# Kernel tuning notes

Hardware: AMD Instinct MI355X
Metric: run time of the kernel (lower is better)

## Reference

```python
import jax, jax.numpy as jnp
import numpy as np

B, T, LATENT, D, N_ENVS = 128, 64, 16, 512, 4
TOPK_RATIO = 0.1
TEMPERATURE = 1.0


def setup_inputs() -> dict:
    key = jax.random.key(0)
    k1, k2, k3, k4 = jax.random.split(key, 4)
    z_s = jax.random.normal(k1, (B, T, LATENT), dtype=jnp.float32)
    env_idx = jax.random.randint(k2, (B,), 0, N_ENVS, dtype=jnp.int64 if jax.config.jax_enable_x64 else jnp.int32)
    A_base = jax.random.normal(k3, (D, D), dtype=jnp.float32) * 0.1
    A_deltas = jax.random.normal(k4, (N_ENVS, D, D), dtype=jnp.float32) * 0.01  # stacked ParameterList
    return {"z_s": z_s, "env_idx": env_idx, "A_base": A_base, "A_deltas": A_deltas}


def reference(z_s, env_idx, A_base, A_deltas):
    b = z_s.shape[0]
    d = A_base.shape[0]
    # Per-env delta add: the torch loop sums delta_e * (env_idx==e) over envs,
    # which (one env per sample) equals a gather of A_deltas at env_idx.
    A_logits = A_base[None, :, :] + A_deltas[env_idx]          # [B, d, d]
    A_soft = jax.nn.sigmoid(A_logits / TEMPERATURE)            # [B, d, d]
    # Batched top-k sparsification (replaces the per-sample python loop).
    k = max(1, int(TOPK_RATIO * d * d))
    flat = A_logits.reshape(b, d * d)                          # [B, d*d]
    topk_vals, topk_idx = jax.lax.top_k(flat, k)               # [B, k]
    rows = jnp.arange(b)[:, None]                              # [B, 1]
    A_flat = jnp.zeros_like(flat).at[rows, topk_idx].set(jax.nn.sigmoid(topk_vals))
    A = A_flat.reshape(b, d, d)
    return A, A_logits, A_soft
```

## Files before the change

kernel.cpp:

```cpp
#include <hip/hip_runtime.h>
#include <stdint.h>

#define D_DIM   512
#define DD      262144
#define DD4     65536
#define B_DIM   128
#define N_ENVS  4
#define K_SEL   26214
#define BDD     33554432u
#define NBLK    64
#define CAP2    65536
#define CAP3    4096

typedef float nfloat4 __attribute__((ext_vector_type(4)));

#define PK_OFF      64
#define CNT_OFF     128
#define HISTP_OFF   4096
#define HISTP_BYTES (NBLK * N_ENVS * 256 * 4)
#define PAIRS_OFF   (512 * 1024)
#define PAIRS_BYTES ((size_t)N_ENVS * CAP2 * 8)
#define SEL_NEED    (PAIRS_OFF + PAIRS_BYTES)

__device__ __forceinline__ uint32_t fkey(float f) {
    uint32_t u = __float_as_uint(f);
    return (u & 0x80000000u) ? ~u : (u | 0x80000000u);
}
__device__ __forceinline__ float sigmoidf_(float x) {
    return 1.0f / (1.0f + __expf(-x));
}

__global__ __launch_bounds__(256) void hist8_kernel(
    const float* __restrict__ base, const float* __restrict__ deltas,
    uint32_t* __restrict__ histp, uint32_t* __restrict__ cnt8)
{
    int e = blockIdx.y;
    const float4* b4 = (const float4*)base;
    const float4* d4 = (const float4*)(deltas + (size_t)e * DD);
    __shared__ uint32_t s_h[256];
    int tid = threadIdx.x;
    s_h[tid] = 0;
    if (blockIdx.x == 0 && tid == 0) cnt8[e] = 0;
    __syncthreads();
    int g0 = blockIdx.x * 256 + tid;
    #pragma unroll
    for (int r = 0; r < 4; ++r) {
        int g = g0 + r * 16384;
        float4 bv = b4[g], dv = d4[g];
        atomicAdd(&s_h[fkey(bv.x + dv.x) >> 24], 1u);
        atomicAdd(&s_h[fkey(bv.y + dv.y) >> 24], 1u);
        atomicAdd(&s_h[fkey(bv.z + dv.z) >> 24], 1u);
        atomicAdd(&s_h[fkey(bv.w + dv.w) >> 24], 1u);
    }
    __syncthreads();
    histp[(blockIdx.x * N_ENVS + e) * 256 + tid] = s_h[tid];
}

__global__ __launch_bounds__(256) void gather8_kernel(
    const float* __restrict__ base, const float* __restrict__ deltas,
    const uint32_t* __restrict__ histp, uint32_t* __restrict__ pk,
    uint32_t* __restrict__ cnt8, uint2* __restrict__ pairs8)
{
    int e = blockIdx.y;
    const float4* b4 = (const float4*)base;
    const float4* d4 = (const float4*)(deltas + (size_t)e * DD);
    uint2* pp = pairs8 + (size_t)e * CAP2;
    __shared__ uint32_t s_h[256];
    __shared__ uint32_t s_scan[256];
    __shared__ uint32_t s_P, s_base;
    int tid = threadIdx.x;

    uint32_t sum = 0;
    #pragma unroll 8
    for (int j = 0; j < NBLK; ++j)
        sum += histp[(j * N_ENVS + e) * 256 + tid];
    s_h[tid] = sum;
    __syncthreads();
    if (tid == 0) {
        uint32_t cum = 0;
        for (int b = 255; b >= 0; --b) {
            uint32_t c = s_h[b];
            if (cum + c >= (uint32_t)K_SEL) {
                s_P = (uint32_t)b;
                if (blockIdx.x == 0) {
                    pk[2 * e + 0] = (uint32_t)b;
                    pk[2 * e + 1] = (uint32_t)K_SEL - cum;
                }
                break;
            }
            cum += c;
        }
    }
    __syncthreads();
    uint32_t P = s_P;

    int g0 = blockIdx.x * 256 + tid;
    uint32_t keys[16];
    uint32_t m = 0;
    #pragma unroll
    for (int r = 0; r < 4; ++r) {
        int g = g0 + r * 16384;
        float4 bv = b4[g], dv = d4[g];
        uint32_t k0 = fkey(bv.x + dv.x), k1 = fkey(bv.y + dv.y);
        uint32_t k2 = fkey(bv.z + dv.z), k3 = fkey(bv.w + dv.w);
        keys[r * 4 + 0] = k0; keys[r * 4 + 1] = k1;
        keys[r * 4 + 2] = k2; keys[r * 4 + 3] = k3;
        m += ((k0 >> 24) == P) + ((k1 >> 24) == P)
           + ((k2 >> 24) == P) + ((k3 >> 24) == P);
    }
    s_scan[tid] = m;
    __syncthreads();
    #pragma unroll
    for (int off = 1; off < 256; off <<= 1) {
        uint32_t v = (tid >= off) ? s_scan[tid - off] : 0u;
        __syncthreads();
        s_scan[tid] += v;
        __syncthreads();
    }
    uint32_t excl = s_scan[tid] - m;
    if (tid == 255) s_base = atomicAdd(&cnt8[e], s_scan[255]);
    __syncthreads();
    uint32_t pos = s_base + excl;

    #pragma unroll
    for (int r = 0; r < 4; ++r) {
        int g = g0 + r * 16384;
        #pragma unroll
        for (int j = 0; j < 4; ++j) {
            uint32_t key = keys[r * 4 + j];
            if ((key >> 24) == P) {
                if (pos < CAP2) pp[pos] = make_uint2(key, (uint32_t)(g * 4 + j));
                ++pos;
            }
        }
    }
}

__global__ __launch_bounds__(1024) void select2_kernel(
    const uint32_t* __restrict__ pk, const uint32_t* __restrict__ cnt8,
    const uint2* __restrict__ pairs8, uint32_t* __restrict__ thrcut)
{
    int e = blockIdx.x;
    const uint2* pp = pairs8 + (size_t)e * CAP2;
    uint32_t M = cnt8[e]; if (M > CAP2) M = CAP2;
    uint32_t krem8 = pk[2 * e + 1];

    __shared__ uint32_t s_h16[256];
    __shared__ uint2    s_pairs[CAP3];
    __shared__ uint32_t s_b16, s_krem16, s_cnt;
    int tid = threadIdx.x;
    if (tid < 256) s_h16[tid] = 0;
    if (tid == 0) s_cnt = 0;
    __syncthreads();

    for (uint32_t j = tid; j < M; j += 1024)
        atomicAdd(&s_h16[(pp[j].x >> 16) & 255u], 1u);
    __syncthreads();
    if (tid == 0) {
        uint32_t cum = 0;
        for (int b = 255; b >= 0; --b) {
            uint32_t c = s_h16[b];
            if (cum + c >= krem8) { s_b16 = (uint32_t)b; s_krem16 = krem8 - cum; break; }
            cum += c;
        }
    }
    __syncthreads();
    uint32_t b16 = s_b16;
    for (uint32_t j = tid; j < M; j += 1024) {
        uint2 p = pp[j];
        if (((p.x >> 16) & 255u) == b16) {
            uint32_t pos = atomicAdd(&s_cnt, 1u);
            if (pos < CAP3) s_pairs[pos] = p;
        }
    }
    __syncthreads();
    uint32_t M2 = s_cnt; if (M2 > CAP3) M2 = CAP3;
    uint32_t target = s_krem16 - 1;
    for (uint32_t j = tid; j < M2; j += 1024) {
        uint2 me = s_pairs[j];
        uint32_t rank = 0;
        for (uint32_t l = 0; l < M2; ++l) {
            uint2 o = s_pairs[l];
            rank += (o.x > me.x) || (o.x == me.x && o.y < me.y);
        }
        if (rank == target) {
            thrcut[2 * e + 0] = me.x;
            thrcut[2 * e + 1] = me.y;
        }
    }
}

__global__ __launch_bounds__(256) void fused_write_kernel(
    const int* __restrict__ env_idx, const float* __restrict__ base,
    const float* __restrict__ deltas, const uint32_t* __restrict__ thrcut,
    float* __restrict__ out)
{
    int b = blockIdx.y;
    int e = env_idx[b];
    uint32_t T = thrcut[2 * e], C = thrcut[2 * e + 1];
    const float4* b4 = (const float4*)base;
    const float4* d4 = (const float4*)(deltas + (size_t)e * DD);
    nfloat4* o4 = (nfloat4*)out + (size_t)b * DD4;
    int g0 = blockIdx.x * 512 + threadIdx.x;
    #pragma unroll
    for (int r = 0; r < 2; ++r) {
        int g = g0 + r * 256;
        uint32_t i0 = (uint32_t)g * 4u;
        float4 bv = b4[g];
        float4 dv = d4[g];
        nfloat4 lg = { bv.x + dv.x, bv.y + dv.y, bv.z + dv.z, bv.w + dv.w };
        nfloat4 sg = { sigmoidf_(lg.x), sigmoidf_(lg.y),
                       sigmoidf_(lg.z), sigmoidf_(lg.w) };
        uint32_t kx = fkey(lg.x), ky = fkey(lg.y), kz = fkey(lg.z), kw = fkey(lg.w);
        nfloat4 av;
        av.x = (kx > T || (kx == T && i0 + 0u <= C)) ? sg.x : 0.0f;
        av.y = (ky > T || (ky == T && i0 + 1u <= C)) ? sg.y : 0.0f;
        av.z = (kz > T || (kz == T && i0 + 2u <= C)) ? sg.z : 0.0f;
        av.w = (kw > T || (kw == T && i0 + 3u <= C)) ? sg.w : 0.0f;
        __builtin_nontemporal_store(av, o4 + g);
        __builtin_nontemporal_store(lg, o4 + g + (BDD / 4));
        __builtin_nontemporal_store(sg, o4 + g + 2ull * (BDD / 4));
    }
}

extern "C" void kernel_launch(void* const* d_in, const int* in_sizes, int n_in,
                              void* d_out, int out_size, void* d_ws, size_t ws_size,
                              hipStream_t stream) {
    const int*   env_idx  = (const int*)d_in[1];
    const float* A_base   = (const float*)d_in[2];
    const float* A_deltas = (const float*)d_in[3];
    float* out = (float*)d_out;

    uint32_t* thrcut = (uint32_t*)d_ws;

    char* scratch;
    if (ws_size >= SEL_NEED) {
        scratch = (char*)d_ws;
    } else {
        size_t out_bytes = (size_t)out_size * sizeof(float);
        scratch = (char*)d_out + ((out_bytes - SEL_NEED) & ~(size_t)255);
    }
    uint32_t* pk     = (uint32_t*)(scratch + PK_OFF);
    uint32_t* cnt8   = (uint32_t*)(scratch + CNT_OFF);
    uint32_t* histp  = (uint32_t*)(scratch + HISTP_OFF);
    uint2*    pairs8 = (uint2*)   (scratch + PAIRS_OFF);

    hist8_kernel  <<<dim3(NBLK, N_ENVS), 256, 0, stream>>>(A_base, A_deltas,
                                                           histp, cnt8);
    gather8_kernel<<<dim3(NBLK, N_ENVS), 256, 0, stream>>>(A_base, A_deltas, histp,
                                                           pk, cnt8, pairs8);
    select2_kernel<<<N_ENVS, 1024, 0, stream>>>(pk, cnt8, pairs8, thrcut);
    fused_write_kernel<<<dim3(DD4 / 512, B_DIM), 256, 0, stream>>>(
        env_idx, A_base, A_deltas, thrcut, out);
}
```

Before: 461.6 us.

## Compute per-env outputs once per element and broadcast to batch rows

The write kernel now computes logits, sigmoid and the masked top-k values for all four environments once per element, then writes them to 16 batch rows per block by switching on env_idx. Before, each of the 128 batch rows reloaded and recomputed its environment's values. The stores switch from nontemporal to regular stores, and the grid becomes 256x8 with a 16-row loop. CAP2 is also enlarged, which raises the scratch footprint. Because the kernel is dominated by 400MB of writes, the savings in reads and compute may matter little, and losing the nontemporal hint could hurt.

```diff
diff --git a/kernel.cpp b/kernel.cpp
--- a/kernel.cpp
+++ b/kernel.cpp
@@ -9,7 +9,7 @@
 #define K_SEL   26214
 #define BDD     33554432u
 #define NBLK    64
-#define CAP2    65536
+#define CAP2    98304
 #define CAP3    4096
 
 typedef float nfloat4 __attribute__((ext_vector_type(4)));
@@ -17,7 +17,6 @@
 #define PK_OFF      64
 #define CNT_OFF     128
 #define HISTP_OFF   4096
-#define HISTP_BYTES (NBLK * N_ENVS * 256 * 4)
 #define PAIRS_OFF   (512 * 1024)
 #define PAIRS_BYTES ((size_t)N_ENVS * CAP2 * 8)
 #define SEL_NEED    (PAIRS_OFF + PAIRS_BYTES)
@@ -190,36 +189,47 @@
     }
 }
 
-__global__ __launch_bounds__(256) void fused_write_kernel(
+__global__ __launch_bounds__(256) void write_bcast_kernel(
     const int* __restrict__ env_idx, const float* __restrict__ base,
     const float* __restrict__ deltas, const uint32_t* __restrict__ thrcut,
     float* __restrict__ out)
 {
-    int b = blockIdx.y;
-    int e = env_idx[b];
-    uint32_t T = thrcut[2 * e], C = thrcut[2 * e + 1];
-    const float4* b4 = (const float4*)base;
-    const float4* d4 = (const float4*)(deltas + (size_t)e * DD);
-    nfloat4* o4 = (nfloat4*)out + (size_t)b * DD4;
-    int g0 = blockIdx.x * 512 + threadIdx.x;
-    #pragma unroll
-    for (int r = 0; r < 2; ++r) {
-        int g = g0 + r * 256;
-        uint32_t i0 = (uint32_t)g * 4u;
-        float4 bv = b4[g];
-        float4 dv = d4[g];
+    int g = blockIdx.x * 256 + threadIdx.x;
+    uint32_t i0 = (uint32_t)g * 4u;
+    float4 bv = ((const float4*)base)[g];
+
+    nfloat4 lgv[N_ENVS], sgv[N_ENVS], avv[N_ENVS];
+    #pragma unroll
+    for (int e = 0; e < N_ENVS; ++e) {
+        float4 dv = ((const float4*)(deltas + (size_t)e * DD))[g];
+        uint32_t T = thrcut[2 * e], C = thrcut[2 * e + 1];
         nfloat4 lg = { bv.x + dv.x, bv.y + dv.y, bv.z + dv.z, bv.w + dv.w };
         nfloat4 sg = { sigmoidf_(lg.x), sigmoidf_(lg.y),
                        sigmoidf_(lg.z), sigmoidf_(lg.w) };
-        uint32_t kx = fkey(lg.x), ky = fkey(lg.y), kz = fkey(lg.z), kw = fkey(lg.w);
+        uint32_t kx = fkey(lg.x), ky = fkey(lg.y);
+        uint32_t kz = fkey(lg.z), kw = fkey(lg.w);
         nfloat4 av;
         av.x = (kx > T || (kx == T && i0 + 0u <= C)) ? sg.x : 0.0f;
         av.y = (ky > T || (ky == T && i0 + 1u <= C)) ? sg.y : 0.0f;
         av.z = (kz > T || (kz == T && i0 + 2u <= C)) ? sg.z : 0.0f;
         av.w = (kw > T || (kw == T && i0 + 3u <= C)) ? sg.w : 0.0f;
-        __builtin_nontemporal_store(av, o4 + g);
-        __builtin_nontemporal_store(lg, o4 + g + (BDD / 4));
-        __builtin_nontemporal_store(sg, o4 + g + 2ull * (BDD / 4));
+        lgv[e] = lg; sgv[e] = sg; avv[e] = av;
+    }
+
+    const int ROWS = B_DIM / 8;
+    int b0 = blockIdx.y * ROWS;
+    nfloat4* o0 = (nfloat4*)out + g;
+    #pragma unroll 4
+    for (int bb = 0; bb < ROWS; ++bb) {
+        int b = b0 + bb;
+        int e = env_idx[b];
+        nfloat4* o = o0 + (size_t)b * DD4;
+        switch (e) {
+        case 0: o[0] = avv[0]; o[BDD/4] = lgv[0]; o[2*(BDD/4)] = sgv[0]; break;
+        case 1: o[0] = avv[1]; o[BDD/4] = lgv[1]; o[2*(BDD/4)] = sgv[1]; break;
+        case 2: o[0] = avv[2]; o[BDD/4] = lgv[2]; o[2*(BDD/4)] = sgv[2]; break;
+        default: o[0] = avv[3]; o[BDD/4] = lgv[3]; o[2*(BDD/4)] = sgv[3]; break;
+        }
     }
 }
 
@@ -250,6 +260,6 @@
     gather8_kernel<<<dim3(NBLK, N_ENVS), 256, 0, stream>>>(A_base, A_deltas, histp,
                                                            pk, cnt8, pairs8);
     select2_kernel<<<N_ENVS, 1024, 0, stream>>>(pk, cnt8, pairs8, thrcut);
-    fused_write_kernel<<<dim3(DD4 / 512, B_DIM), 256, 0, stream>>>(
+    write_bcast_kernel<<<dim3(DD4 / 256, 8), 256, 0, stream>>>(
         env_idx, A_base, A_deltas, thrcut, out);
 }
```

Measured after the change: 456.3 us. About the same (-1.1%).
